# Optimization experiments

Hardware: AMD Instinct MI355X
Metric: run time of the kernel (lower is better)

Reference implementation:

```python
import jax, jax.numpy as jnp
import numpy as np

EPS = 1e-5

def conv2d(x, w, stride=1, padding=0, bias=None):
    out = jax.lax.conv_general_dilated(
        x, w, (stride, stride), [(padding, padding), (padding, padding)],
        dimension_numbers=('NCHW', 'OIHW', 'NCHW'))
    if bias is not None:
        out = out + bias[None, :, None, None]
    return out

def bn_relu(x, gamma, beta, mean, var):
    scale = gamma / jnp.sqrt(var + EPS)
    return jax.nn.relu(x * scale[None, :, None, None]
                       + (beta - mean * scale)[None, :, None, None])

def deform_conv(x, wp, bp, wc, ks, pad, stride):
    # Canonical DeformConv2d (v1, modulation=False) from pytorch-deform-conv-v2.
    b, c, H, W = x.shape
    N = ks * ks
    offset = conv2d(x, wp, stride=stride, padding=1, bias=bp)        # (b,2N,h,w)
    h, w = offset.shape[2], offset.shape[3]
    xp = jnp.pad(x, ((0, 0), (0, 0), (pad, pad), (pad, pad)))        # zero_padding
    Hp, Wp = H + 2 * pad, W + 2 * pad
    off = offset.transpose(0, 2, 3, 1)                               # (b,h,w,2N)
    rng = jnp.arange(-(ks - 1) // 2, (ks - 1) // 2 + 1, dtype=x.dtype)
    pnx, pny = jnp.meshgrid(rng, rng, indexing='ij')
    pnx, pny = pnx.reshape(-1), pny.reshape(-1)                      # (N,)
    p0x = jnp.arange(1, h * stride + 1, stride, dtype=x.dtype)       # torch starts at 1
    p0y = jnp.arange(1, w * stride + 1, stride, dtype=x.dtype)
    px = p0x[None, :, None, None] + pnx[None, None, None, :] + off[..., :N]  # (b,h,w,N)
    py = p0y[None, None, :, None] + pny[None, None, None, :] + off[..., N:]
    qx0 = jnp.floor(jax.lax.stop_gradient(px))
    qy0 = jnp.floor(jax.lax.stop_gradient(py))
    qx0c = jnp.clip(qx0, 0, Hp - 1).astype(jnp.int32)
    qx1c = jnp.clip(qx0 + 1, 0, Hp - 1).astype(jnp.int32)
    qy0c = jnp.clip(qy0, 0, Wp - 1).astype(jnp.int32)
    qy1c = jnp.clip(qy0 + 1, 0, Wp - 1).astype(jnp.int32)
    pxc = jnp.clip(px, 0, Hp - 1)
    pyc = jnp.clip(py, 0, Wp - 1)
    fx0 = qx0c.astype(x.dtype); fx1 = qx1c.astype(x.dtype)
    fy0 = qy0c.astype(x.dtype); fy1 = qy1c.astype(x.dtype)
    g_lt = (1 + (fx0 - pxc)) * (1 + (fy0 - pyc))
    g_rb = (1 - (fx1 - pxc)) * (1 - (fy1 - pyc))
    g_lb = (1 + (fx0 - pxc)) * (1 - (fy1 - pyc))
    g_rt = (1 - (fx1 - pxc)) * (1 + (fy0 - pyc))
    xf = xp.reshape(b, c, Hp * Wp)
    def gather(qx, qy):
        idx = (qx * Wp + qy).reshape(b, 1, h * w * N)
        return jnp.take_along_axis(xf, idx, axis=2).reshape(b, c, h, w, N)
    x_off = (g_lt[:, None] * gather(qx0c, qy0c)
             + g_rb[:, None] * gather(qx1c, qy1c)
             + g_lb[:, None] * gather(qx0c, qy1c)
             + g_rt[:, None] * gather(qx1c, qy0c))                   # (b,c,h,w,N)
    # stride=ks conv over the reshaped (h*ks, w*ks) map == einsum over sample slot n
    return jnp.einsum('bchwn,ocn->bohw', x_off, wc.reshape(wc.shape[0], c, N))

def setup_inputs() -> dict:
    key = jax.random.key(0)
    ks = iter(jax.random.split(key, 40))
    def nrm(shape, scale):
        return jax.random.normal(next(ks), shape, dtype=jnp.float32) * scale
    def he(shape):  # fan_in = prod of all but first dim
        return nrm(shape, float(np.sqrt(2.0 / np.prod(shape[1:]))))
    def bn(c):
        return (jnp.ones((c,), jnp.float32) + nrm((c,), 0.05),  # gamma
                nrm((c,), 0.05),                                 # beta
                nrm((c,), 0.1),                                  # running mean
                jax.random.uniform(next(ks), (c,), jnp.float32, 0.5, 1.5))  # var
    inp = {'x': jax.random.normal(next(ks), (256, 3, 32, 32), dtype=jnp.float32)}
    inp['w1'] = he((32, 3, 3, 3)); inp['b1'] = nrm((32,), 0.01)
    inp['g1'], inp['be1'], inp['m1'], inp['v1'] = bn(32)
    inp['wp2'] = nrm((18, 32, 3, 3), 0.01); inp['bp2'] = nrm((18,), 0.001)
    inp['wc2'] = he((64, 32, 3, 3))
    inp['g2'], inp['be2'], inp['m2'], inp['v2'] = bn(64)
    inp['wp3'] = nrm((18, 64, 3, 3), 0.01); inp['bp3'] = nrm((18,), 0.001)
    inp['wc3'] = he((128, 64, 3, 3))
    inp['g3'], inp['be3'], inp['m3'], inp['v3'] = bn(128)
    inp['wp4'] = nrm((18, 128, 3, 3), 0.01); inp['bp4'] = nrm((18,), 0.001)
    inp['wc4'] = he((128, 128, 3, 3))
    inp['g4'], inp['be4'], inp['m4'], inp['v4'] = bn(128)
    inp['wcls'] = nrm((100, 128), float(1.0 / np.sqrt(128)))
    inp['bcls'] = nrm((100,), 0.01)
    return inp

def reference(x, w1, b1, g1, be1, m1, v1,
              wp2, bp2, wc2, g2, be2, m2, v2,
              wp3, bp3, wc3, g3, be3, m3, v3,
              wp4, bp4, wc4, g4, be4, m4, v4,
              wcls, bcls):
    h = bn_relu(conv2d(x, w1, stride=1, padding=1, bias=b1), g1, be1, m1, v1)   # (b,32,32,32)
    h = bn_relu(deform_conv(h, wp2, bp2, wc2, 3, 1, 2), g2, be2, m2, v2)        # (b,64,16,16)
    h = bn_relu(deform_conv(h, wp3, bp3, wc3, 3, 1, 1), g3, be3, m3, v3)        # (b,128,16,16)
    h = bn_relu(deform_conv(h, wp4, bp4, wc4, 3, 1, 2), g4, be4, m4, v4)        # (b,128,8,8)
    h = jnp.mean(h, axis=(2, 3))                                                # avg_pool2d(8) -> (b,128)
    return h @ wcls.T + bcls[None, :]
```

## Files before the change

kernel.cpp:

```cpp
#include <hip/hip_runtime.h>
#include <math.h>

#define BN_EPS 1e-5f

typedef __attribute__((ext_vector_type(4))) float f4;
typedef __attribute__((ext_vector_type(4))) int i4v;
typedef __attribute__((ext_vector_type(8))) short short8;
typedef __attribute__((ext_vector_type(4))) float f32x4;
typedef _Float16 half4v __attribute__((ext_vector_type(4)));

__device__ inline unsigned short f2bf(float f) {
    unsigned int u = __builtin_bit_cast(unsigned int, f);
    return (unsigned short)((u + 0x7FFFu + ((u >> 16) & 1u)) >> 16);
}
__device__ inline float blo(int u) { return __builtin_bit_cast(float, (int)(u << 16)); }
__device__ inline float bhi(int u) { return __builtin_bit_cast(float, (int)(u & 0xffff0000)); }
__device__ inline int pkbf_fast(float hi, float lo) {
    unsigned uh = __builtin_bit_cast(unsigned, hi) + 0x8000u;
    unsigned ul = __builtin_bit_cast(unsigned, lo) + 0x8000u;
    return (int)__builtin_amdgcn_perm(uh, ul, 0x07060302u);
}

struct CvtSeg { const float* src; unsigned short* dst; int oreal, c, kpad, end; };
struct CvtArgs { CvtSeg s[7]; };

__global__ __launch_bounds__(256)
void cvt_all(CvtArgs a)
{
    int idx = blockIdx.x * 256 + threadIdx.x;
    int base = 0;
    #pragma unroll
    for (int i = 0; i < 7; ++i) {
        if (idx < a.s[i].end) {
            int local = idx - base;
            int kpad = a.s[i].kpad, c = a.s[i].c;
            int o = local / kpad, k = local - o * kpad;
            unsigned short val = 0;
            if (o < a.s[i].oreal && k < 9 * c) {
                int n = k / c, cc = k - n * c;
                val = f2bf(a.s[i].src[(o * c + cc) * 9 + n]);
            }
            a.s[i].dst[local] = val;
            return;
        }
        base = a.s[i].end;
    }
}

__global__ __launch_bounds__(256)
void conv1_tile(const float* __restrict__ x, const unsigned short* __restrict__ wq,
                const float* __restrict__ bias, const float* __restrict__ g,
                const float* __restrict__ be, const float* __restrict__ m,
                const float* __restrict__ v, unsigned short* __restrict__ out)
{
    __shared__ __align__(16) float img[3072];
    __shared__ __align__(16) unsigned short wt[32 * 40];
    __shared__ float scb[32], shb[32];
    const int tid = threadIdx.x;
    const int b = blockIdx.x >> 2;
    const int qtr = blockIdx.x & 3;
    if (tid < 32) {
        float sc = g[tid] * rsqrtf(v[tid] + BN_EPS);
        scb[tid] = sc;
        shb[tid] = be[tid] - m[tid] * sc + bias[tid] * sc;
    }
    *(ushort4*)&wt[(tid >> 3) * 40 + (tid & 7) * 4] =
        *(const ushort4*)(wq + (tid >> 3) * 32 + (tid & 7) * 4);
    const float* xb = x + (size_t)b * 3072;
    #pragma unroll
    for (int r = 0; r < 3; ++r) {
        int idx = r * 256 + tid;
        *(f4*)&img[idx * 4] = *(const f4*)(xb + idx * 4);
    }
    __syncthreads();
    const int wid = tid >> 6, lane = tid & 63, quad = lane >> 4, m16 = lane & 15;
    short8 af0 = *(const short8*)&wt[m16 * 40 + quad * 8];
    short8 af1 = *(const short8*)&wt[(16 + m16) * 40 + quad * 8];
    #pragma unroll
    for (int it = 0; it < 4; ++it) {
        int pix = qtr * 256 + it * 64 + wid * 16 + m16;
        int i = pix >> 5, j = pix & 31;
        short8 bfrag;
        #pragma unroll
        for (int jj = 0; jj < 8; ++jj) {
            int k = quad * 8 + jj;
            float val = 0.f;
            if (k < 27) {
                int n = k / 3, c = k - n * 3;
                int u = i - 1 + n / 3, vv = j - 1 + n % 3;
                if (u >= 0 && u < 32 && vv >= 0 && vv < 32)
                    val = img[c * 1024 + u * 32 + vv];
            }
            bfrag[jj] = (short)f2bf(val);
        }
        f32x4 a0 = {0.f,0.f,0.f,0.f}, a1 = {0.f,0.f,0.f,0.f};
        a0 = __builtin_amdgcn_mfma_f32_16x16x32_bf16(af0, bfrag, a0, 0, 0, 0);
        a1 = __builtin_amdgcn_mfma_f32_16x16x32_bf16(af1, bfrag, a1, 0, 0, 0);
        unsigned short* op = out + ((size_t)b * 1024 + pix) * 32;
        ushort4 s0, s1;
        #pragma unroll
        for (int rr = 0; rr < 4; ++rr) {
            int o0 = quad * 4 + rr, o1 = 16 + quad * 4 + rr;
            ((unsigned short*)&s0)[rr] = f2bf(fmaxf(fmaf(a0[rr], scb[o0], shb[o0]), 0.f));
            ((unsigned short*)&s1)[rr] = f2bf(fmaxf(fmaf(a1[rr], scb[o1], shb[o1]), 0.f));
        }
        *(ushort4*)(op + quad * 4) = s0;
        *(ushort4*)(op + 16 + quad * 4) = s1;
    }
}

template<int C, int OREAL, int OPAD, int H, int W, int OH, int OW, int S,
         int MTILE, int OBLK>
__global__ __launch_bounds__(256, 4)
void dconv_fused(const unsigned short* __restrict__ xact,
                 const unsigned short* __restrict__ wp, const float* __restrict__ bp,
                 const unsigned short* __restrict__ wc,
                 const float* __restrict__ g, const float* __restrict__ be,
                 const float* __restrict__ m, const float* __restrict__ v,
                 unsigned short* __restrict__ out)
{
    constexpr int K = C * 9;
    constexpr int KCH = C / 32;
    constexpr int OPB = OPAD / OBLK;
    constexpr int OT = OPB / 64;
    constexpr int ST = MTILE / 16;
    constexpr int PWP = (MTILE >= 32) ? MTILE / 2 : MTILE;
    constexpr int STP = PWP / 16;
    constexpr int CP = C + 8;
    constexpr int GL = C / 8;
    constexpr int NGRP = 256 / GL;
    constexpr int NT = MTILE / NGRP;
    constexpr int OHW = OH * OW;
    constexpr int HWC = H * W * C;
    constexpr int Hp = H + 2, Wpp = W + 2;
    static_assert(MTILE % NGRP == 0 && OPB % 64 == 0 && STP >= 1, "tiling");

    __shared__ __align__(16) unsigned short xo[2][MTILE * CP];
    __shared__ __align__(8) ushort4   tab_p[MTILE][9];
    __shared__ __align__(8) _Float16  tab_h[MTILE][9][4];
    __shared__ _Float16 off_lds[MTILE][20];
    __shared__ int imgb[MTILE];
    __shared__ float scb[OPAD], shb[OPAD];

    const int tid = threadIdx.x;
    const int ob  = blockIdx.x % OBLK;
    const int p0  = (blockIdx.x / OBLK) * MTILE;

    if (tid < MTILE) imgb[tid] = ((p0 + tid) / OHW) * HWC;
    for (int o = tid; o < OREAL; o += 256) {
        float sc = g[o] * rsqrtf(v[o] + BN_EPS);
        scb[o] = sc;
        shb[o] = be[o] - m[o] * sc;
    }
    for (int e = tid; e < MTILE * 9; e += 256) {
        int lp = e / 9, n = e % 9;
        int p = p0 + lp;
        int rem = p % OHW;
        int i = rem / OW, j = rem % OW;
        int u = i * S - 1 + n / 3, vv = j * S - 1 + n % 3;
        bool ok = (u >= 0 && u < H && vv >= 0 && vv < W);
        ushort4 tp;
        tp.x = ok ? (unsigned short)((u * W + vv) * C) : (unsigned short)0;
        tp.y = ok ? (unsigned short)0xFFFF : (unsigned short)0;
        tp.z = 0; tp.w = 0;
        tab_p[lp][n] = tp;
    }
    __syncthreads();

    const int gl = tid % GL, grp = tid / GL;
    const int wid = tid >> 6, lane = tid & 63, quad = lane >> 4, m16 = lane & 15;

    {
        const int ogp = wid & 1;
        const int pgp = (MTILE >= 32) ? (wid >> 1) : 0;
        const int obp = ogp * 16;
        const int pbp = pgp * PWP;
        i4v Tp[NT];
        auto issueA = [&](int n) {
            #pragma unroll
            for (int it = 0; it < NT; ++it) {
                const int pix = it * NGRP + grp;
                Tp[it] = *(const i4v*)(xact + imgb[pix] + gl * 8 + (int)tab_p[pix][n].x);
            }
        };
        auto commitA = [&](int n, int buf) {
            #pragma unroll
            for (int it = 0; it < NT; ++it) {
                const int pix = it * NGRP + grp;
                int mask = (int)(short)tab_p[pix][n].y;
                i4v R;
                #pragma unroll
                for (int e2 = 0; e2 < 4; ++e2) R[e2] = Tp[it][e2] & mask;
                *(i4v*)&xo[buf][pix * CP + gl * 8] = R;
            }
        };
        auto loadWp = [&](int n, short8* wf) {
            #pragma unroll
            for (int ch = 0; ch < KCH; ++ch)
                wf[ch] = *(const short8*)(wp + (size_t)(obp + m16) * K
                                          + n * C + ch * 32 + quad * 8);
        };
        f32x4 accp[STP];
        #pragma unroll
        for (int st = 0; st < STP; ++st) accp[st] = (f32x4){0.f, 0.f, 0.f, 0.f};
        short8 wfA[KCH], wfB[KCH];
        issueA(0);
        loadWp(0, wfA);
        commitA(0, 0);
        __syncthreads();
        for (int n = 0; n < 9; ++n) {
            const int cur = n & 1;
            if (n < 8) { issueA(n + 1); loadWp(n + 1, wfB); }
            #pragma unroll
            for (int ch = 0; ch < KCH; ++ch)
                #pragma unroll
                for (int st = 0; st < STP; ++st) {
                    short8 bf = *(const short8*)&xo[cur][(pbp + st * 16 + m16) * CP
                                                        + ch * 32 + quad * 8];
                    accp[st] = __builtin_amdgcn_mfma_f32_16x16x32_bf16(
                        wfA[ch], bf, accp[st], 0, 0, 0);
                }
            if (n < 8) {
                commitA(n + 1, cur ^ 1);
                #pragma unroll
                for (int ch = 0; ch < KCH; ++ch) wfA[ch] = wfB[ch];
            }
            __syncthreads();
        }
        #pragma unroll
        for (int st = 0; st < STP; ++st) {
            int pix = pbp + st * 16 + m16;
            #pragma unroll
            for (int rr = 0; rr < 4; ++rr) {
                int o = obp + quad * 4 + rr;
                if (o < 18) off_lds[pix][o] = (_Float16)(accp[st][rr] + bp[o]);
            }
        }
    }
    __syncthreads();

    for (int e = tid; e < MTILE * 9; e += 256) {
        int lp = e / 9, n = e % 9;
        int p = p0 + lp;
        int rem = p % OHW;
        int i = rem / OW, j = rem % OW;
        float ox = (float)off_lds[lp][n];
        float oy = (float)off_lds[lp][9 + n];
        float px = (float)(i * S + n / 3) + ox;
        float py = (float)(j * S + n % 3) + oy;
        int qx0 = (int)floorf(px), qy0 = (int)floorf(py);
        int x0 = min(max(qx0, 0), Hp - 1), x1 = min(max(qx0 + 1, 0), Hp - 1);
        int y0 = min(max(qy0, 0), Wpp - 1), y1 = min(max(qy0 + 1, 0), Wpp - 1);
        float pxc = fminf(fmaxf(px, 0.f), (float)(Hp - 1));
        float pyc = fminf(fmaxf(py, 0.f), (float)(Wpp - 1));
        float gx0 = 1.f + ((float)x0 - pxc), gx1 = 1.f - ((float)x1 - pxc);
        float gy0 = 1.f + ((float)y0 - pyc), gy1 = 1.f - ((float)y1 - pyc);
        int u0 = x0 - 1, u1 = x1 - 1, v0 = y0 - 1, v1 = y1 - 1;
        bool k0 = (u0 >= 0 && u0 < H && v0 >= 0 && v0 < W);
        bool k1 = (u1 >= 0 && u1 < H && v1 >= 0 && v1 < W);
        bool k2 = (u0 >= 0 && u0 < H && v1 >= 0 && v1 < W);
        bool k3 = (u1 >= 0 && u1 < H && v0 >= 0 && v0 < W);
        ushort4 tp;
        tp.x = k0 ? (unsigned short)((u0 * W + v0) * C) : (unsigned short)0;
        tp.y = k1 ? (unsigned short)((u1 * W + v1) * C) : (unsigned short)0;
        tp.z = k2 ? (unsigned short)((u0 * W + v1) * C) : (unsigned short)0;
        tp.w = k3 ? (unsigned short)((u1 * W + v0) * C) : (unsigned short)0;
        tab_p[lp][n] = tp;
        half4v hw;
        hw[0] = (_Float16)(k0 ? gx0 * gy0 : 0.f);
        hw[1] = (_Float16)(k1 ? gx1 * gy1 : 0.f);
        hw[2] = (_Float16)(k2 ? gx0 * gy1 : 0.f);
        hw[3] = (_Float16)(k3 ? gx1 * gy0 : 0.f);
        *(half4v*)&tab_h[lp][n][0] = hw;
    }
    __syncthreads();

    {
        const int obase = ob * OPB + wid * OT * 16;
        i4v T[NT][4];
        auto issueC = [&](int n) {
            #pragma unroll
            for (int it = 0; it < NT; ++it) {
                const int pix = it * NGRP + grp;
                const unsigned short* xb = xact + imgb[pix] + gl * 8;
                ushort4 tp = tab_p[pix][n];
                T[it][0] = *(const i4v*)(xb + tp.x);
                T[it][1] = *(const i4v*)(xb + tp.y);
                T[it][2] = *(const i4v*)(xb + tp.z);
                T[it][3] = *(const i4v*)(xb + tp.w);
            }
        };
        auto commitC = [&](int n, int buf) {
            #pragma unroll
            for (int it = 0; it < NT; ++it) {
                const int pix = it * NGRP + grp;
                half4v hw = *(const half4v*)&tab_h[pix][n][0];
                float w0 = (float)hw[0], w1 = (float)hw[1];
                float w2 = (float)hw[2], w3 = (float)hw[3];
                i4v R;
                #pragma unroll
                for (int e2 = 0; e2 < 4; ++e2) {
                    float lo = w0 * blo(T[it][0][e2]);
                    lo = fmaf(w1, blo(T[it][1][e2]), lo);
                    lo = fmaf(w2, blo(T[it][2][e2]), lo);
                    lo = fmaf(w3, blo(T[it][3][e2]), lo);
                    float hi = w0 * bhi(T[it][0][e2]);
                    hi = fmaf(w1, bhi(T[it][1][e2]), hi);
                    hi = fmaf(w2, bhi(T[it][2][e2]), hi);
                    hi = fmaf(w3, bhi(T[it][3][e2]), hi);
                    R[e2] = pkbf_fast(hi, lo);
                }
                *(i4v*)&xo[buf][pix * CP + gl * 8] = R;
            }
        };
        auto loadWc = [&](int n, short8 (*wf)[OT]) {
            #pragma unroll
            for (int ch = 0; ch < KCH; ++ch)
                #pragma unroll
                for (int t = 0; t < OT; ++t)
                    wf[ch][t] = *(const short8*)(wc + (size_t)(obase + t * 16 + m16) * K
                                                 + n * C + ch * 32 + quad * 8);
        };

        f32x4 acc[ST][OT];
        #pragma unroll
        for (int st = 0; st < ST; ++st)
            #pragma unroll
            for (int t = 0; t < OT; ++t) acc[st][t] = (f32x4){0.f, 0.f, 0.f, 0.f};

        short8 wfA[KCH][OT], wfB[KCH][OT];
        issueC(0);
        loadWc(0, wfA);
        commitC(0, 0);
        __syncthreads();

        for (int n = 0; n < 9; ++n) {
            const int cur = n & 1;
            if (n < 8) {
                issueC(n + 1);
                loadWc(n + 1, wfB);
            }
            #pragma unroll
            for (int ch = 0; ch < KCH; ++ch)
                #pragma unroll
                for (int st = 0; st < ST; ++st) {
                    short8 bf = *(const short8*)&xo[cur][(st * 16 + m16) * CP
                                                        + ch * 32 + quad * 8];
                    #pragma unroll
                    for (int t = 0; t < OT; ++t)
                        acc[st][t] = __builtin_amdgcn_mfma_f32_16x16x32_bf16(
                            wfA[ch][t], bf, acc[st][t], 0, 0, 0);
                }
            if (n < 8) {
                commitC(n + 1, cur ^ 1);
                #pragma unroll
                for (int ch = 0; ch < KCH; ++ch)
                    #pragma unroll
                    for (int t = 0; t < OT; ++t) wfA[ch][t] = wfB[ch][t];
            }
            __syncthreads();
        }

        #pragma unroll
        for (int st = 0; st < ST; ++st) {
            const int p = p0 + st * 16 + m16;
            #pragma unroll
            for (int t = 0; t < OT; ++t) {
                int o = obase + t * 16 + quad * 4;
                ushort4 s;
                #pragma unroll
                for (int rr = 0; rr < 4; ++rr)
                    ((unsigned short*)&s)[rr] =
                        f2bf(fmaxf(fmaf(acc[st][t][rr], scb[o + rr], shb[o + rr]), 0.f));
                *(ushort4*)(out + (size_t)p * OPAD + o) = s;
            }
        }
    }
}

template<int C, int O, int H, int W, int OH, int OW, int S>
__global__ __launch_bounds__(256, 2)
void dconv_img(const unsigned short* __restrict__ xact,
               const unsigned short* __restrict__ wp, const float* __restrict__ bp,
               const unsigned short* __restrict__ wc,
               const float* __restrict__ g, const float* __restrict__ be,
               const float* __restrict__ m, const float* __restrict__ v,
               unsigned short* __restrict__ out)
{
    constexpr int K = C * 9;
    constexpr int KCH = C / 32;
    constexpr int NPIX = OH * OW;
    constexpr int ST = NPIX / 16;
    constexpr int HWC = H * W * C;
    constexpr int Hp = H + 2, Wpp = W + 2;

    __shared__ __align__(16) unsigned short img[HWC];
    __shared__ _Float16 off_lds[NPIX][20];
    __shared__ float scb[O], shb[O];

    const int tid = threadIdx.x;
    const int b  = blockIdx.x >> 1;
    const int ob = blockIdx.x & 1;

    const unsigned short* srcim = xact + (size_t)b * HWC;
    #pragma unroll
    for (int it = 0; it < HWC / 2048; ++it) {
        int idx = (it * 256 + tid) * 8;
        *(i4v*)&img[idx] = *(const i4v*)(srcim + idx);
    }
    for (int o = tid; o < O; o += 256) {
        float sc = g[o] * rsqrtf(v[o] + BN_EPS);
        scb[o] = sc;
        shb[o] = be[o] - m[o] * sc;
    }
    __syncthreads();

    const int wid = tid >> 6, lane = tid & 63, quad = lane >> 4, m16 = lane & 15;

    {
        const int pl = wid * 16 + m16;
        const int i = pl / OW, j = pl % OW;
        f32x4 accp[2] = {{0.f,0.f,0.f,0.f},{0.f,0.f,0.f,0.f}};
        short8 wfA[KCH][2], wfB[KCH][2];
        auto loadWp = [&](int n, short8 (*wf)[2]) {
            #pragma unroll
            for (int ch = 0; ch < KCH; ++ch)
                #pragma unroll
                for (int t = 0; t < 2; ++t)
                    wf[ch][t] = *(const short8*)(wp + (size_t)(t * 16 + m16) * K
                                                 + n * C + ch * 32 + quad * 8);
        };
        loadWp(0, wfA);
        for (int n = 0; n < 9; ++n) {
            if (n < 8) loadWp(n + 1, wfB);
            int u = i * S - 1 + n / 3, vv = j * S - 1 + n % 3;
            bool ok = (u >= 0 && u < H && vv >= 0 && vv < W);
            int ta = ok ? (u * W + vv) * C : 0;
            int mask = ok ? -1 : 0;
            #pragma unroll
            for (int ch = 0; ch < KCH; ++ch) {
                i4v A = *(const i4v*)&img[ta + ch * 32 + quad * 8];
                i4v R;
                #pragma unroll
                for (int e2 = 0; e2 < 4; ++e2) R[e2] = A[e2] & mask;
                short8 bf = __builtin_bit_cast(short8, R);
                accp[0] = __builtin_amdgcn_mfma_f32_16x16x32_bf16(wfA[ch][0], bf, accp[0], 0, 0, 0);
                accp[1] = __builtin_amdgcn_mfma_f32_16x16x32_bf16(wfA[ch][1], bf, accp[1], 0, 0, 0);
            }
            if (n < 8) {
                #pragma unroll
                for (int ch = 0; ch < KCH; ++ch) {
                    wfA[ch][0] = wfB[ch][0];
                    wfA[ch][1] = wfB[ch][1];
                }
            }
        }
        #pragma unroll
        for (int t = 0; t < 2; ++t)
            #pragma unroll
            for (int rr = 0; rr < 4; ++rr) {
                int o = t * 16 + quad * 4 + rr;
                if (o < 18) off_lds[pl][o] = (_Float16)(accp[t][rr] + bp[o]);
            }
    }
    __syncthreads();

    {
        const int obase = ob * (O / 2) + wid * 16;
        f32x4 acc[ST];
        #pragma unroll
        for (int st = 0; st < ST; ++st) acc[st] = (f32x4){0.f, 0.f, 0.f, 0.f};
        short8 wfA[KCH], wfB[KCH];
        auto loadWc = [&](int n, short8* wf) {
            #pragma unroll
            for (int ch = 0; ch < KCH; ++ch)
                wf[ch] = *(const short8*)(wc + (size_t)(obase + m16) * K
                                          + n * C + ch * 32 + quad * 8);
        };
        loadWc(0, wfA);
        for (int n = 0; n < 9; ++n) {
            if (n < 8) loadWc(n + 1, wfB);
            #pragma unroll
            for (int st = 0; st < ST; ++st) {
                const int pl = st * 16 + m16;
                const int i = pl / OW, j = pl % OW;
                float ox = (float)off_lds[pl][n];
                float oy = (float)off_lds[pl][9 + n];
                float px = (float)(i * S + n / 3) + ox;
                float py = (float)(j * S + n % 3) + oy;
                int qx0 = (int)floorf(px), qy0 = (int)floorf(py);
                int x0 = min(max(qx0, 0), Hp - 1), x1 = min(max(qx0 + 1, 0), Hp - 1);
                int y0 = min(max(qy0, 0), Wpp - 1), y1 = min(max(qy0 + 1, 0), Wpp - 1);
                float pxc = fminf(fmaxf(px, 0.f), (float)(Hp - 1));
                float pyc = fminf(fmaxf(py, 0.f), (float)(Wpp - 1));
                float gx0 = 1.f + ((float)x0 - pxc), gx1 = 1.f - ((float)x1 - pxc);
                float gy0 = 1.f + ((float)y0 - pyc), gy1 = 1.f - ((float)y1 - pyc);
                int u0 = x0 - 1, u1 = x1 - 1, v0 = y0 - 1, v1 = y1 - 1;
                bool k0 = (u0 >= 0 && u0 < H && v0 >= 0 && v0 < W);
                bool k1 = (u1 >= 0 && u1 < H && v1 >= 0 && v1 < W);
                bool k2 = (u0 >= 0 && u0 < H && v1 >= 0 && v1 < W);
                bool k3 = (u1 >= 0 && u1 < H && v0 >= 0 && v0 < W);
                int t0 = k0 ? (u0 * W + v0) * C : 0;  float w0 = k0 ? gx0 * gy0 : 0.f;
                int t1 = k1 ? (u1 * W + v1) * C : 0;  float w1 = k1 ? gx1 * gy1 : 0.f;
                int t2 = k2 ? (u0 * W + v1) * C : 0;  float w2 = k2 ? gx0 * gy1 : 0.f;
                int t3 = k3 ? (u1 * W + v0) * C : 0;  float w3 = k3 ? gx1 * gy0 : 0.f;
                #pragma unroll
                for (int ch = 0; ch < KCH; ++ch) {
                    const int cb = ch * 32 + quad * 8;
                    i4v A  = *(const i4v*)&img[t0 + cb];
                    i4v Bv = *(const i4v*)&img[t1 + cb];
                    i4v Cv = *(const i4v*)&img[t2 + cb];
                    i4v Dv = *(const i4v*)&img[t3 + cb];
                    i4v R;
                    #pragma unroll
                    for (int e2 = 0; e2 < 4; ++e2) {
                        float lo = w0 * blo(A[e2]);
                        lo = fmaf(w1, blo(Bv[e2]), lo);
                        lo = fmaf(w2, blo(Cv[e2]), lo);
                        lo = fmaf(w3, blo(Dv[e2]), lo);
                        float hi = w0 * bhi(A[e2]);
                        hi = fmaf(w1, bhi(Bv[e2]), hi);
                        hi = fmaf(w2, bhi(Cv[e2]), hi);
                        hi = fmaf(w3, bhi(Dv[e2]), hi);
                        R[e2] = pkbf_fast(hi, lo);
                    }
                    short8 bf = __builtin_bit_cast(short8, R);
                    acc[st] = __builtin_amdgcn_mfma_f32_16x16x32_bf16(wfA[ch], bf, acc[st], 0, 0, 0);
                }
            }
            if (n < 8) {
                #pragma unroll
                for (int ch = 0; ch < KCH; ++ch) wfA[ch] = wfB[ch];
            }
        }
        #pragma unroll
        for (int st = 0; st < ST; ++st) {
            const int pl = st * 16 + m16;
            int o = obase + quad * 4;
            ushort4 s;
            #pragma unroll
            for (int rr = 0; rr < 4; ++rr)
                ((unsigned short*)&s)[rr] =
                    f2bf(fmaxf(fmaf(acc[st][rr], scb[o + rr], shb[o + rr]), 0.f));
            *(ushort4*)(out + ((size_t)b * NPIX + pl) * O + o) = s;
        }
    }
}

__global__ __launch_bounds__(128)
void pool_fc(const unsigned short* __restrict__ h4, const float* __restrict__ wcls,
             const float* __restrict__ bcls, float* __restrict__ out)
{
    __shared__ float pool[128];
    int b = blockIdx.x;
    int tid = threadIdx.x;
    const unsigned short* src = h4 + (size_t)b * 8192;
    float s = 0.f;
    #pragma unroll
    for (int t = 0; t < 64; ++t)
        s += __builtin_bit_cast(float, (unsigned)src[t * 128 + tid] << 16);
    pool[tid] = s * (1.f / 64.f);
    __syncthreads();
    if (tid < 100) {
        float acc = bcls[tid];
        const float* wr = wcls + tid * 128;
        #pragma unroll
        for (int c = 0; c < 128; ++c) acc = fmaf(pool[c], wr[c], acc);
        out[(size_t)b * 100 + tid] = acc;
    }
}

extern "C" void kernel_launch(void* const* d_in, const int* in_sizes, int n_in,
                              void* d_out, int out_size, void* d_ws, size_t ws_size,
                              hipStream_t stream)
{
    const float* x    = (const float*)d_in[0];
    const float* w1   = (const float*)d_in[1];
    const float* b1   = (const float*)d_in[2];
    const float* g1   = (const float*)d_in[3];
    const float* be1  = (const float*)d_in[4];
    const float* m1   = (const float*)d_in[5];
    const float* v1   = (const float*)d_in[6];
    const float* wp2  = (const float*)d_in[7];
    const float* bp2  = (const float*)d_in[8];
    const float* wc2  = (const float*)d_in[9];
    const float* g2   = (const float*)d_in[10];
    const float* be2  = (const float*)d_in[11];
    const float* m2   = (const float*)d_in[12];
    const float* v2   = (const float*)d_in[13];
    const float* wp3  = (const float*)d_in[14];
    const float* bp3  = (const float*)d_in[15];
    const float* wc3  = (const float*)d_in[16];
    const float* g3   = (const float*)d_in[17];
    const float* be3  = (const float*)d_in[18];
    const float* m3   = (const float*)d_in[19];
    const float* v3   = (const float*)d_in[20];
    const float* wp4  = (const float*)d_in[21];
    const float* bp4  = (const float*)d_in[22];
    const float* wc4  = (const float*)d_in[23];
    const float* g4   = (const float*)d_in[24];
    const float* be4  = (const float*)d_in[25];
    const float* m4   = (const float*)d_in[26];
    const float* v4   = (const float*)d_in[27];
    const float* wcls = (const float*)d_in[28];
    const float* bcls = (const float*)d_in[29];
    float* out = (float*)d_out;

    unsigned short* h1 = (unsigned short*)d_ws;
    unsigned short* h2 = h1 + 8388608;
    unsigned short* h3 = h2 + 4194304;
    unsigned short* h4 = h3 + 8388608;
    unsigned short* wc2b = h4 + 2097152;
    unsigned short* wc3b = wc2b + 18432;
    unsigned short* wc4b = wc3b + 73728;
    unsigned short* wp2b = wc4b + 147456;
    unsigned short* wp3b = wp2b + 9216;
    unsigned short* wp4b = wp3b + 18432;
    unsigned short* wq1  = wp4b + 36864;
    (void)ws_size; (void)in_sizes; (void)n_in; (void)out_size;

    CvtArgs ca;
    ca.s[0] = { wc2, wc2b, 64, 32, 288, 18432 };
    ca.s[1] = { wc3, wc3b, 128, 64, 576, 92160 };
    ca.s[2] = { wc4, wc4b, 128, 128, 1152, 239616 };
    ca.s[3] = { wp2, wp2b, 18, 32, 288, 248832 };
    ca.s[4] = { wp3, wp3b, 18, 64, 576, 267264 };
    ca.s[5] = { wp4, wp4b, 18, 128, 1152, 304128 };
    ca.s[6] = { w1, wq1, 32, 3, 32, 305152 };
    cvt_all<<<1192, 256, 0, stream>>>(ca);

    conv1_tile<<<1024, 256, 0, stream>>>(x, wq1, b1, g1, be1, m1, v1, h1);

    dconv_fused<32, 64, 64, 32, 32, 16, 16, 2, 64, 1><<<1024, 256, 0, stream>>>(
        h1, wp2b, bp2, wc2b, g2, be2, m2, v2, h2);

    dconv_fused<64, 128, 128, 16, 16, 16, 16, 1, 64, 1><<<1024, 256, 0, stream>>>(
        h2, wp3b, bp3, wc3b, g3, be3, m3, v3, h3);

    dconv_img<128, 128, 16, 16, 8, 8, 2><<<512, 256, 0, stream>>>(
        h3, wp4b, bp4, wc4b, g4, be4, m4, v4, h4);

    pool_fc<<<256, 128, 0, stream>>>(h4, wcls, bcls, out);
}
```

Baseline: 282.0 us.

## Replace per-image layer-4 deform conv with pixel-tiled double-buffered LDS pipeline

The last deformable conv layer no longer copies a whole 16x16x128 image into LDS per block and computes sampling coordinates inline. It now tiles 32 output pixels per block. Offsets, bilinear indices and weights are precomputed into fp32 LDS tables, and the sampled, interpolated activations are staged into double-buffered LDS tiles fed to MFMA, overlapping global gathers with compute. The first two layers drop the unused OBLK template parameter. In exchange, layer 4 gathers directly from global memory instead of from a resident LDS image, which may raise memory traffic.

```diff
diff --git a/kernel.cpp b/kernel.cpp
--- a/kernel.cpp
+++ b/kernel.cpp
@@ -109,22 +109,20 @@
     }
 }
 
-template<int C, int OREAL, int OPAD, int H, int W, int OH, int OW, int S,
-         int MTILE, int OBLK>
+template<int C, int OREAL, int OPAD, int H, int W, int OH, int OW, int S, int MTILE>
 __global__ __launch_bounds__(256, 4)
-void dconv_fused(const unsigned short* __restrict__ xact,
-                 const unsigned short* __restrict__ wp, const float* __restrict__ bp,
-                 const unsigned short* __restrict__ wc,
-                 const float* __restrict__ g, const float* __restrict__ be,
-                 const float* __restrict__ m, const float* __restrict__ v,
-                 unsigned short* __restrict__ out)
+void dconv_slim(const unsigned short* __restrict__ xact,
+                const unsigned short* __restrict__ wp, const float* __restrict__ bp,
+                const unsigned short* __restrict__ wc,
+                const float* __restrict__ g, const float* __restrict__ be,
+                const float* __restrict__ m, const float* __restrict__ v,
+                unsigned short* __restrict__ out)
 {
     constexpr int K = C * 9;
     constexpr int KCH = C / 32;
-    constexpr int OPB = OPAD / OBLK;
-    constexpr int OT = OPB / 64;
+    constexpr int OT = OPAD / 64;
     constexpr int ST = MTILE / 16;
-    constexpr int PWP = (MTILE >= 32) ? MTILE / 2 : MTILE;
+    constexpr int PWP = MTILE / 2;
     constexpr int STP = PWP / 16;
     constexpr int CP = C + 8;
     constexpr int GL = C / 8;
@@ -133,7 +131,7 @@
     constexpr int OHW = OH * OW;
     constexpr int HWC = H * W * C;
     constexpr int Hp = H + 2, Wpp = W + 2;
-    static_assert(MTILE % NGRP == 0 && OPB % 64 == 0 && STP >= 1, "tiling");
+    static_assert(MTILE % NGRP == 0 && OPAD % 64 == 0 && STP >= 1, "tiling");
 
     __shared__ __align__(16) unsigned short xo[2][MTILE * CP];
     __shared__ __align__(8) ushort4   tab_p[MTILE][9];
@@ -143,8 +141,7 @@
     __shared__ float scb[OPAD], shb[OPAD];
 
     const int tid = threadIdx.x;
-    const int ob  = blockIdx.x % OBLK;
-    const int p0  = (blockIdx.x / OBLK) * MTILE;
+    const int p0 = blockIdx.x * MTILE;
 
     if (tid < MTILE) imgb[tid] = ((p0 + tid) / OHW) * HWC;
     for (int o = tid; o < OREAL; o += 256) {
@@ -172,7 +169,7 @@
 
     {
         const int ogp = wid & 1;
-        const int pgp = (MTILE >= 32) ? (wid >> 1) : 0;
+        const int pgp = wid >> 1;
         const int obp = ogp * 16;
         const int pbp = pgp * PWP;
         i4v Tp[NT];
@@ -276,7 +273,7 @@
     __syncthreads();
 
     {
-        const int obase = ob * OPB + wid * OT * 16;
+        const int obase = wid * OT * 16;
         i4v T[NT][4];
         auto issueC = [&](int n) {
             #pragma unroll
@@ -378,9 +375,9 @@
     }
 }
 
-template<int C, int O, int H, int W, int OH, int OW, int S>
-__global__ __launch_bounds__(256, 2)
-void dconv_img(const unsigned short* __restrict__ xact,
+template<int C, int OREAL, int OPAD, int H, int W, int OH, int OW, int S, int MTILE>
+__global__ __launch_bounds__(256, 3)
+void dconv_fat(const unsigned short* __restrict__ xact,
                const unsigned short* __restrict__ wp, const float* __restrict__ bp,
                const unsigned short* __restrict__ wc,
                const float* __restrict__ g, const float* __restrict__ be,
@@ -389,160 +386,248 @@
 {
     constexpr int K = C * 9;
     constexpr int KCH = C / 32;
-    constexpr int NPIX = OH * OW;
-    constexpr int ST = NPIX / 16;
+    constexpr int OT = OPAD / 64;
+    constexpr int ST = MTILE / 16;
+    constexpr int PWP = MTILE / 2;
+    constexpr int STP = PWP / 16;
+    constexpr int CP = C + 8;
+    constexpr int GL = C / 8;
+    constexpr int NGRP = 256 / GL;
+    constexpr int NT = MTILE / NGRP;
+    constexpr int OHW = OH * OW;
     constexpr int HWC = H * W * C;
     constexpr int Hp = H + 2, Wpp = W + 2;
-
-    __shared__ __align__(16) unsigned short img[HWC];
-    __shared__ _Float16 off_lds[NPIX][20];
-    __shared__ float scb[O], shb[O];
+    static_assert(MTILE % NGRP == 0 && OPAD % 64 == 0, "tiling");
+
+    __shared__ __align__(16) unsigned short xo[2][MTILE * CP];
+    __shared__ __align__(16) i4v tab_i[MTILE][9];
+    __shared__ __align__(16) f4  tab_w[MTILE][9];
+    __shared__ int tab_o[MTILE][9];
+    __shared__ int tab_m[MTILE][9];
+    __shared__ float off_lds[MTILE][20];
+    __shared__ int imgb[MTILE];
+    __shared__ float scb[OPAD], shb[OPAD];
 
     const int tid = threadIdx.x;
-    const int b  = blockIdx.x >> 1;
-    const int ob = blockIdx.x & 1;
-
-    const unsigned short* srcim = xact + (size_t)b * HWC;
-    #pragma unroll
-    for (int it = 0; it < HWC / 2048; ++it) {
-        int idx = (it * 256 + tid) * 8;
-        *(i4v*)&img[idx] = *(const i4v*)(srcim + idx);
-    }
-    for (int o = tid; o < O; o += 256) {
+    const int p0 = blockIdx.x * MTILE;
+
+    if (tid < MTILE) imgb[tid] = ((p0 + tid) / OHW) * HWC;
+    for (int o = tid; o < OREAL; o += 256) {
         float sc = g[o] * rsqrtf(v[o] + BN_EPS);
         scb[o] = sc;
         shb[o] = be[o] - m[o] * sc;
     }
+    for (int e = tid; e < MTILE * 9; e += 256) {
+        int lp = e / 9, n = e % 9;
+        int p = p0 + lp;
+        int rem = p % OHW;
+        int i = rem / OW, j = rem % OW;
+        int u = i * S - 1 + n / 3, vv = j * S - 1 + n % 3;
+        bool ok = (u >= 0 && u < H && vv >= 0 && vv < W);
+        tab_o[lp][n] = ok ? (u * W + vv) * C : 0;
+        tab_m[lp][n] = ok ? -1 : 0;
+    }
     __syncthreads();
 
+    const int gl = tid % GL, grp = tid / GL;
     const int wid = tid >> 6, lane = tid & 63, quad = lane >> 4, m16 = lane & 15;
 
     {
-        const int pl = wid * 16 + m16;
-        const int i = pl / OW, j = pl % OW;
-        f32x4 accp[2] = {{0.f,0.f,0.f,0.f},{0.f,0.f,0.f,0.f}};
-        short8 wfA[KCH][2], wfB[KCH][2];
-        auto loadWp = [&](int n, short8 (*wf)[2]) {
+        const int ogp = wid & 1, pgp = wid >> 1;
+        const int obp = ogp * 16;
+        const int pbp = pgp * PWP;
+        i4v Tp[NT];
+        auto issueA = [&](int n) {
+            #pragma unroll
+            for (int it = 0; it < NT; ++it) {
+                const int pix = it * NGRP + grp;
+                Tp[it] = *(const i4v*)(xact + imgb[pix] + gl * 8 + tab_o[pix][n]);
+            }
+        };
+        auto commitA = [&](int n, int buf) {
+            #pragma unroll
+            for (int it = 0; it < NT; ++it) {
+                const int pix = it * NGRP + grp;
+                int mask = tab_m[pix][n];
+                i4v R;
+                #pragma unroll
+                for (int e2 = 0; e2 < 4; ++e2) R[e2] = Tp[it][e2] & mask;
+                *(i4v*)&xo[buf][pix * CP + gl * 8] = R;
+            }
+        };
+        auto loadWp = [&](int n, short8* wf) {
             #pragma unroll
             for (int ch = 0; ch < KCH; ++ch)
-                #pragma unroll
-                for (int t = 0; t < 2; ++t)
-                    wf[ch][t] = *(const short8*)(wp + (size_t)(t * 16 + m16) * K
+                wf[ch] = *(const short8*)(wp + (size_t)(obp + m16) * K
+                                          + n * C + ch * 32 + quad * 8);
+        };
+        f32x4 accp[STP];
+        #pragma unroll
+        for (int st = 0; st < STP; ++st) accp[st] = (f32x4){0.f, 0.f, 0.f, 0.f};
+        short8 wfA[KCH], wfB[KCH];
+        issueA(0);
+        loadWp(0, wfA);
+        commitA(0, 0);
+        __syncthreads();
+        for (int n = 0; n < 9; ++n) {
+            const int cur = n & 1;
+            if (n < 8) { issueA(n + 1); loadWp(n + 1, wfB); }
+            #pragma unroll
+            for (int ch = 0; ch < KCH; ++ch)
+                #pragma unroll
+                for (int st = 0; st < STP; ++st) {
+                    short8 bf = *(const short8*)&xo[cur][(pbp + st * 16 + m16) * CP
+                                                        + ch * 32 + quad * 8];
+                    accp[st] = __builtin_amdgcn_mfma_f32_16x16x32_bf16(
+                        wfA[ch], bf, accp[st], 0, 0, 0);
+                }
+            if (n < 8) {
+                commitA(n + 1, cur ^ 1);
+                #pragma unroll
+                for (int ch = 0; ch < KCH; ++ch) wfA[ch] = wfB[ch];
+            }
+            __syncthreads();
+        }
+        #pragma unroll
+        for (int st = 0; st < STP; ++st) {
+            int pix = pbp + st * 16 + m16;
+            #pragma unroll
+            for (int rr = 0; rr < 4; ++rr) {
+                int o = obp + quad * 4 + rr;
+                if (o < 18) off_lds[pix][o] = accp[st][rr] + bp[o];
+            }
+        }
+    }
+    __syncthreads();
+
+    for (int e = tid; e < MTILE * 9; e += 256) {
+        int lp = e / 9, n = e % 9;
+        int p = p0 + lp;
+        int rem = p % OHW;
+        int i = rem / OW, j = rem % OW;
+        float ox = off_lds[lp][n];
+        float oy = off_lds[lp][9 + n];
+        float px = (float)(i * S + n / 3) + ox;
+        float py = (float)(j * S + n % 3) + oy;
+        int qx0 = (int)floorf(px), qy0 = (int)floorf(py);
+        int x0 = min(max(qx0, 0), Hp - 1), x1 = min(max(qx0 + 1, 0), Hp - 1);
+        int y0 = min(max(qy0, 0), Wpp - 1), y1 = min(max(qy0 + 1, 0), Wpp - 1);
+        float pxc = fminf(fmaxf(px, 0.f), (float)(Hp - 1));
+        float pyc = fminf(fmaxf(py, 0.f), (float)(Wpp - 1));
+        float gx0 = 1.f + ((float)x0 - pxc), gx1 = 1.f - ((float)x1 - pxc);
+        float gy0 = 1.f + ((float)y0 - pyc), gy1 = 1.f - ((float)y1 - pyc);
+        int u0 = x0 - 1, u1 = x1 - 1, v0 = y0 - 1, v1 = y1 - 1;
+        bool k0 = (u0 >= 0 && u0 < H && v0 >= 0 && v0 < W);
+        bool k1 = (u1 >= 0 && u1 < H && v1 >= 0 && v1 < W);
+        bool k2 = (u0 >= 0 && u0 < H && v1 >= 0 && v1 < W);
+        bool k3 = (u1 >= 0 && u1 < H && v0 >= 0 && v0 < W);
+        i4v ti; f4 tw;
+        ti[0] = k0 ? (u0 * W + v0) * C : 0;  tw[0] = k0 ? gx0 * gy0 : 0.f;
+        ti[1] = k1 ? (u1 * W + v1) * C : 0;  tw[1] = k1 ? gx1 * gy1 : 0.f;
+        ti[2] = k2 ? (u0 * W + v1) * C : 0;  tw[2] = k2 ? gx0 * gy1 : 0.f;
+        ti[3] = k3 ? (u1 * W + v0) * C : 0;  tw[3] = k3 ? gx1 * gy0 : 0.f;
+        tab_i[lp][n] = ti;
+        tab_w[lp][n] = tw;
+    }
+    __syncthreads();
+
+    {
+        const int obase = wid * OT * 16;
+        i4v T[NT][4];
+        auto issueC = [&](int n) {
+            #pragma unroll
+            for (int it = 0; it < NT; ++it) {
+                const int pix = it * NGRP + grp;
+                const unsigned short* xb = xact + imgb[pix] + gl * 8;
+                i4v ti = tab_i[pix][n];
+                T[it][0] = *(const i4v*)(xb + ti[0]);
+                T[it][1] = *(const i4v*)(xb + ti[1]);
+                T[it][2] = *(const i4v*)(xb + ti[2]);
+                T[it][3] = *(const i4v*)(xb + ti[3]);
+            }
+        };
+        auto commitC = [&](int n, int buf) {
+            #pragma unroll
+            for (int it = 0; it < NT; ++it) {
+                const int pix = it * NGRP + grp;
+                f4 tw = tab_w[pix][n];
+                i4v R;
+                #pragma unroll
+                for (int e2 = 0; e2 < 4; ++e2) {
+                    float lo = tw[0] * blo(T[it][0][e2]);
+                    lo = fmaf(tw[1], blo(T[it][1][e2]), lo);
+                    lo = fmaf(tw[2], blo(T[it][2][e2]), lo);
+                    lo = fmaf(tw[3], blo(T[it][3][e2]), lo);
+                    float hi = tw[0] * bhi(T[it][0][e2]);
+                    hi = fmaf(tw[1], bhi(T[it][1][e2]), hi);
+                    hi = fmaf(tw[2], bhi(T[it][2][e2]), hi);
+                    hi = fmaf(tw[3], bhi(T[it][3][e2]), hi);
+                    R[e2] = pkbf_fast(hi, lo);
+                }
+                *(i4v*)&xo[buf][pix * CP + gl * 8] = R;
+            }
+        };
+        auto loadWc = [&](int n, short8 (*wf)[OT]) {
+            #pragma unroll
+            for (int ch = 0; ch < KCH; ++ch)
+                #pragma unroll
+                for (int t = 0; t < OT; ++t)
+                    wf[ch][t] = *(const short8*)(wc + (size_t)(obase + t * 16 + m16) * K
                                                  + n * C + ch * 32 + quad * 8);
         };
-        loadWp(0, wfA);
+
+        f32x4 acc[ST][OT];
+        #pragma unroll
+        for (int st = 0; st < ST; ++st)
+            #pragma unroll
+            for (int t = 0; t < OT; ++t) acc[st][t] = (f32x4){0.f, 0.f, 0.f, 0.f};
+
+        short8 wfA[KCH][OT], wfB[KCH][OT];
+        issueC(0);
+        loadWc(0, wfA);
+        commitC(0, 0);
+        __syncthreads();
+
         for (int n = 0; n < 9; ++n) {
-            if (n < 8) loadWp(n + 1, wfB);
-            int u = i * S - 1 + n / 3, vv = j * S - 1 + n % 3;
-            bool ok = (u >= 0 && u < H && vv >= 0 && vv < W);
-            int ta = ok ? (u * W + vv) * C : 0;
-            int mask = ok ? -1 : 0;
-            #pragma unroll
-            for (int ch = 0; ch < KCH; ++ch) {
-                i4v A = *(const i4v*)&img[ta + ch * 32 + quad * 8];
-                i4v R;
-                #pragma unroll
-                for (int e2 = 0; e2 < 4; ++e2) R[e2] = A[e2] & mask;
-                short8 bf = __builtin_bit_cast(short8, R);
-                accp[0] = __builtin_amdgcn_mfma_f32_16x16x32_bf16(wfA[ch][0], bf, accp[0], 0, 0, 0);
-                accp[1] = __builtin_amdgcn_mfma_f32_16x16x32_bf16(wfA[ch][1], bf, accp[1], 0, 0, 0);
-            }
+            const int cur = n & 1;
             if (n < 8) {
-                #pragma unroll
-                for (int ch = 0; ch < KCH; ++ch) {
-                    wfA[ch][0] = wfB[ch][0];
-                    wfA[ch][1] = wfB[ch][1];
+                issueC(n + 1);
+                loadWc(n + 1, wfB);
+            }
+            #pragma unroll
+            for (int ch = 0; ch < KCH; ++ch)
+                #pragma unroll
+                for (int st = 0; st < ST; ++st) {
+                    short8 bf = *(const short8*)&xo[cur][(st * 16 + m16) * CP
+                                                        + ch * 32 + quad * 8];
+                    #pragma unroll
+                    for (int t = 0; t < OT; ++t)
+                        acc[st][t] = __builtin_amdgcn_mfma_f32_16x16x32_bf16(
+                            wfA[ch][t], bf, acc[st][t], 0, 0, 0);
                 }
-            }
-        }
-        #pragma unroll
-        for (int t = 0; t < 2; ++t)
-            #pragma unroll
-            for (int rr = 0; rr < 4; ++rr) {
-                int o = t * 16 + quad * 4 + rr;
-                if (o < 18) off_lds[pl][o] = (_Float16)(accp[t][rr] + bp[o]);
-            }
-    }
-    __syncthreads();
-
-    {
-        const int obase = ob * (O / 2) + wid * 16;
-        f32x4 acc[ST];
-        #pragma unroll
-        for (int st = 0; st < ST; ++st) acc[st] = (f32x4){0.f, 0.f, 0.f, 0.f};
-        short8 wfA[KCH], wfB[KCH];
-        auto loadWc = [&](int n, short8* wf) {
-            #pragma unroll
-            for (int ch = 0; ch < KCH; ++ch)
-                wf[ch] = *(const short8*)(wc + (size_t)(obase + m16) * K
-                                          + n * C + ch * 32 + quad * 8);
-        };
-        loadWc(0, wfA);
-        for (int n = 0; n < 9; ++n) {
-            if (n < 8) loadWc(n + 1, wfB);
-            #pragma unroll
-            for (int st = 0; st < ST; ++st) {
-                const int pl = st * 16 + m16;
-                const int i = pl / OW, j = pl % OW;
-                float ox = (float)off_lds[pl][n];
-                float oy = (float)off_lds[pl][9 + n];
-                float px = (float)(i * S + n / 3) + ox;
-                float py = (float)(j * S + n % 3) + oy;
-                int qx0 = (int)floorf(px), qy0 = (int)floorf(py);
-                int x0 = min(max(qx0, 0), Hp - 1), x1 = min(max(qx0 + 1, 0), Hp - 1);
-                int y0 = min(max(qy0, 0), Wpp - 1), y1 = min(max(qy0 + 1, 0), Wpp - 1);
-                float pxc = fminf(fmaxf(px, 0.f), (float)(Hp - 1));
-                float pyc = fminf(fmaxf(py, 0.f), (float)(Wpp - 1));
-                float gx0 = 1.f + ((float)x0 - pxc), gx1 = 1.f - ((float)x1 - pxc);
-                float gy0 = 1.f + ((float)y0 - pyc), gy1 = 1.f - ((float)y1 - pyc);
-                int u0 = x0 - 1, u1 = x1 - 1, v0 = y0 - 1, v1 = y1 - 1;
-                bool k0 = (u0 >= 0 && u0 < H && v0 >= 0 && v0 < W);
-                bool k1 = (u1 >= 0 && u1 < H && v1 >= 0 && v1 < W);
-                bool k2 = (u0 >= 0 && u0 < H && v1 >= 0 && v1 < W);
-                bool k3 = (u1 >= 0 && u1 < H && v0 >= 0 && v0 < W);
-                int t0 = k0 ? (u0 * W + v0) * C : 0;  float w0 = k0 ? gx0 * gy0 : 0.f;
-                int t1 = k1 ? (u1 * W + v1) * C : 0;  float w1 = k1 ? gx1 * gy1 : 0.f;
-                int t2 = k2 ? (u0 * W + v1) * C : 0;  float w2 = k2 ? gx0 * gy1 : 0.f;
-                int t3 = k3 ? (u1 * W + v0) * C : 0;  float w3 = k3 ? gx1 * gy0 : 0.f;
-                #pragma unroll
-                for (int ch = 0; ch < KCH; ++ch) {
-                    const int cb = ch * 32 + quad * 8;
-                    i4v A  = *(const i4v*)&img[t0 + cb];
-                    i4v Bv = *(const i4v*)&img[t1 + cb];
-                    i4v Cv = *(const i4v*)&img[t2 + cb];
-                    i4v Dv = *(const i4v*)&img[t3 + cb];
-                    i4v R;
+            if (n < 8) {
+                commitC(n + 1, cur ^ 1);
+                #pragma unroll
+                for (int ch = 0; ch < KCH; ++ch)
                     #pragma unroll
-                    for (int e2 = 0; e2 < 4; ++e2) {
-                        float lo = w0 * blo(A[e2]);
-                        lo = fmaf(w1, blo(Bv[e2]), lo);
-                        lo = fmaf(w2, blo(Cv[e2]), lo);
-                        lo = fmaf(w3, blo(Dv[e2]), lo);
-                        float hi = w0 * bhi(A[e2]);
-                        hi = fmaf(w1, bhi(Bv[e2]), hi);
-                        hi = fmaf(w2, bhi(Cv[e2]), hi);
-                        hi = fmaf(w3, bhi(Dv[e2]), hi);
-                        R[e2] = pkbf_fast(hi, lo);
-                    }
-                    short8 bf = __builtin_bit_cast(short8, R);
-                    acc[st] = __builtin_amdgcn_mfma_f32_16x16x32_bf16(wfA[ch], bf, acc[st], 0, 0, 0);
-                }
-            }
-            if (n < 8) {
-                #pragma unroll
-                for (int ch = 0; ch < KCH; ++ch) wfA[ch] = wfB[ch];
-            }
-        }
+                    for (int t = 0; t < OT; ++t) wfA[ch][t] = wfB[ch][t];
+            }
+            __syncthreads();
+        }
+
         #pragma unroll
         for (int st = 0; st < ST; ++st) {
-            const int pl = st * 16 + m16;
-            int o = obase + quad * 4;
-            ushort4 s;
-            #pragma unroll
-            for (int rr = 0; rr < 4; ++rr)
-                ((unsigned short*)&s)[rr] =
-                    f2bf(fmaxf(fmaf(acc[st][rr], scb[o + rr], shb[o + rr]), 0.f));
-            *(ushort4*)(out + ((size_t)b * NPIX + pl) * O + o) = s;
+            const int p = p0 + st * 16 + m16;
+            #pragma unroll
+            for (int t = 0; t < OT; ++t) {
+                int o = obase + t * 16 + quad * 4;
+                ushort4 s;
+                #pragma unroll
+                for (int rr = 0; rr < 4; ++rr)
+                    ((unsigned short*)&s)[rr] =
+                        f2bf(fmaxf(fmaf(acc[st][t][rr], scb[o + rr], shb[o + rr]), 0.f));
+                *(ushort4*)(out + (size_t)p * OPAD + o) = s;
+            }
         }
     }
 }
@@ -631,13 +716,13 @@
 
     conv1_tile<<<1024, 256, 0, stream>>>(x, wq1, b1, g1, be1, m1, v1, h1);
 
-    dconv_fused<32, 64, 64, 32, 32, 16, 16, 2, 64, 1><<<1024, 256, 0, stream>>>(
+    dconv_slim<32, 64, 64, 32, 32, 16, 16, 2, 64><<<1024, 256, 0, stream>>>(
         h1, wp2b, bp2, wc2b, g2, be2, m2, v2, h2);
 
-    dconv_fused<64, 128, 128, 16, 16, 16, 16, 1, 64, 1><<<1024, 256, 0, stream>>>(
+    dconv_slim<64, 128, 128, 16, 16, 16, 16, 1, 64><<<1024, 256, 0, stream>>>(
         h2, wp3b, bp3, wc3b, g3, be3, m3, v3, h3);
 
-    dconv_img<128, 128, 16, 16, 8, 8, 2><<<512, 256, 0, stream>>>(
+    dconv_fat<128, 128, 128, 16, 16, 8, 8, 2, 32><<<512, 256, 0, stream>>>(
         h3, wp4b, bp4, wc4b, g4, be4, m4, v4, h4);
 
     pool_fc<<<256, 128, 0, stream>>>(h4, wcls, bcls, out);
```

After: 228.4 us. 19.0% less time.
